# Kernel optimization log

Measured on AMD Instinct MI355X. Metric: run time of the kernel, lower is better.

Reference implementation:

```python
import jax, jax.numpy as jnp
import numpy as np

B, T, D, H, E = 2, 1024, 1024, 4096, 8


def setup_inputs() -> dict:
    key = jax.random.key(0)
    ks = jax.random.split(key, 7)
    s = 0.02  # weight init scale
    return {
        "x": jax.random.normal(ks[0], (B, T, D), jnp.float32),
        "gate_w": jax.random.normal(ks[1], (D, E), jnp.float32) * s,
        "gate_b": jnp.zeros((E,), jnp.float32),
        "w1": jax.random.normal(ks[2], (E, D, H), jnp.float32) * s,
        "b1": jnp.zeros((E, H), jnp.float32),
        "w2": jax.random.normal(ks[3], (E, H, D), jnp.float32) * s,
        "b2": jnp.zeros((E, D), jnp.float32),
    }


def reference(x, gate_w, gate_b, w1, b1, w2, b2):
    b, t, d = x.shape
    e = gate_w.shape[1]
    xt = x.reshape(b * t, d)                      # [N, D]
    logits = xt @ gate_w + gate_b                 # [N, E]
    probs = jax.nn.softmax(logits, axis=-1)
    top_expert = jnp.argmax(probs, axis=-1)       # [N]
    onehot = jax.nn.one_hot(top_expert, e, dtype=x.dtype)  # [N, E]
    # dense per-expert FFN, then combine via top-1 one-hot (same math as masked dispatch)
    h = jax.nn.gelu(jnp.einsum('nd,edh->enh', xt, w1) + b1[:, None, :], approximate=False)  # [E, N, H]
    y = jnp.einsum('enh,ehd->end', h, w2) + b2[:, None, :]                                  # [E, N, D]
    out = jnp.einsum('end,ne->nd', y, onehot).reshape(b, t, d)
    counts = jnp.sum(onehot, axis=0)              # [E], float
    frac = counts / jnp.maximum(counts.sum(), 1.0)
    aux_loss = jnp.mean((frac - 1.0 / e) ** 2)
    return out, aux_loss
```

## Files before the change

### kernel.cpp

```cpp
#include <hip/hip_runtime.h>
#include <stdint.h>

#define N_TOK 2048
#define DDIM 1024
#define HDIM 4096
#define NEXP 8
#define BM 128
#define MAXT 24
#define PADCAP 3072

#define C_COUNTS 0
#define C_CURSOR 8
#define C_PADOFF 16
#define C_TILECNT 25
#define C_TILE_E 32
#define C_TILE_M0 56
#define C_TILE_ROWS 80
#define C_EXPERT 128
#define C_PERM 2176

#define XG_OFF 32768
#define HG_OFF (XG_OFF + PADCAP*DDIM*2)

typedef float f32x4 __attribute__((ext_vector_type(4)));
typedef short s16x8 __attribute__((ext_vector_type(8)));
typedef unsigned int u32;
typedef unsigned short u16;

__device__ __forceinline__ u16 f2bf(float f){
  u32 u = __float_as_uint(f);
  u += 0x7fffu + ((u >> 16) & 1u);
  return (u16)(u >> 16);
}

__device__ __forceinline__ u32 pkbf(float a, float b){
  u32 r; asm("v_cvt_pk_bf16_f32 %0, %1, %2" : "=v"(r) : "v"(a), "v"(b)); return r;
}

__device__ __forceinline__ void gl_lds16(const void* g, void* l){
  __builtin_amdgcn_global_load_lds((const __attribute__((address_space(1))) u32*)g,
                                   (__attribute__((address_space(3))) u32*)l, 16, 0, 0);
}

__global__ __launch_bounds__(256) void gate_kern(
    const float* __restrict__ x, const float* __restrict__ gw,
    const float* __restrict__ gb, int* __restrict__ ctrl)
{
  const int wv = threadIdx.x >> 6, l = threadIdx.x & 63;
  const int n = blockIdx.x * 4 + wv;
  const float* xr = x + (size_t)n * DDIM;
  float acc[NEXP];
  #pragma unroll
  for (int e = 0; e < NEXP; e++) acc[e] = 0.f;
  #pragma unroll 4
  for (int i = 0; i < DDIM/64; i++){
    int k = i*64 + l;
    float xv = xr[k];
    const float* g = gw + (size_t)k * NEXP;
    #pragma unroll
    for (int e = 0; e < NEXP; e++) acc[e] = fmaf(xv, g[e], acc[e]);
  }
  #pragma unroll
  for (int e = 0; e < NEXP; e++){
    #pragma unroll
    for (int off = 32; off > 0; off >>= 1) acc[e] += __shfl_xor(acc[e], off);
  }
  if (l == 0){
    float best = acc[0] + gb[0]; int bi = 0;
    #pragma unroll
    for (int e = 1; e < NEXP; e++){
      float v = acc[e] + gb[e];
      if (v > best){ best = v; bi = e; }
    }
    ctrl[C_EXPERT + n] = bi;
    atomicAdd(&ctrl[C_COUNTS + bi], 1);
  }
}

__global__ void setup_kern(int* __restrict__ ctrl, float* __restrict__ aux_out)
{
  const int t = threadIdx.x;
  for (int i = t; i < PADCAP; i += 256) ctrl[C_PERM + i] = -1;
  if (t == 0){
    int off = 0, tc = 0;
    float aux = 0.f;
    for (int e = 0; e < NEXP; e++){
      int c = ctrl[C_COUNTS + e];
      ctrl[C_PADOFF + e] = off;
      ctrl[C_CURSOR + e] = off;
      int nt = (c + BM - 1) / BM;
      for (int j = 0; j < nt; j++){
        ctrl[C_TILE_E   + tc] = e;
        ctrl[C_TILE_M0  + tc] = off + j*BM;
        ctrl[C_TILE_ROWS+ tc] = min(BM, c - j*BM);
        tc++;
      }
      off += nt * BM;
      float fr = (float)c * (1.f/(float)N_TOK);
      float d = fr - 1.f/(float)NEXP;
      aux += d*d;
    }
    ctrl[C_TILECNT] = tc;
    *aux_out = aux * (1.f/(float)NEXP);
  }
}

__global__ __launch_bounds__(256) void scatter_kern(int* __restrict__ ctrl)
{
  const int n = blockIdx.x * 256 + threadIdx.x;
  const int e = ctrl[C_EXPERT + n];
  const int pos = atomicAdd(&ctrl[C_CURSOR + e], 1);
  ctrl[C_PERM + pos] = n;
}

__global__ __launch_bounds__(256) void xg_kern(
    const float* __restrict__ x, const int* __restrict__ ctrl,
    u16* __restrict__ Xg)
{
  const int slot = blockIdx.x, t = threadIdx.x;
  const int tok = ctrl[C_PERM + slot];
  ushort4 o;
  if (tok >= 0){
    f32x4 v = *(const f32x4*)(x + (size_t)tok*DDIM + t*4);
    o.x = f2bf(v.x); o.y = f2bf(v.y); o.z = f2bf(v.z); o.w = f2bf(v.w);
  } else { o.x = 0; o.y = 0; o.z = 0; o.w = 0; }
  *(ushort4*)(Xg + (size_t)slot*DDIM + t*4) = o;
}

template<int MODE>
__global__ __launch_bounds__(256, (MODE==1) ? 3 : 2) void moe_gemm(
    const u16* __restrict__ Ag, const float* __restrict__ W,
    const float* __restrict__ bias, u16* __restrict__ Hg,
    float* __restrict__ outp, const int* __restrict__ ctrl)
{
  constexpr int K    = (MODE==1) ? DDIM : HDIM;
  constexpr int NN   = (MODE==1) ? HDIM : DDIM;
  constexpr int BN   = (MODE==1) ? 128 : 64;
  constexpr int BK   = (MODE==1) ? 32 : 64;
  constexpr int NF   = BN / 32;
  constexpr int NKK  = BK / 32;
  constexpr int CPR  = BK / 8;
  constexpr int AVM  = (BM*BK)/(256*8);
  constexpr int BCPR = BN / 4;
  constexpr int BVM  = (BK*BN)/(256*4);
  constexpr int NT   = K / BK;

  const int by = blockIdx.y;
  if (by >= ctrl[C_TILECNT]) return;
  const int e    = ctrl[C_TILE_E + by];
  const int m0   = ctrl[C_TILE_M0 + by];
  const int rows = ctrl[C_TILE_ROWS + by];
  const int n0   = blockIdx.x * BN;

  const int tid = threadIdx.x;
  const int w = tid >> 6, l = tid & 63;
  const int wr = w >> 1, wc = w & 1;
  const int lhi = l >> 4, llo = l & 15;

  __shared__ __align__(16) u16   As[2][BM*BK];
  __shared__ __align__(16) float Bs[2][BK*BN];
  __shared__ int perm_s[BM];

  if constexpr (MODE == 2){
    if (tid < BM) perm_s[tid] = ctrl[C_PERM + m0 + tid];
  }

  f32x4 acc[4][NF];
  #pragma unroll
  for (int mf = 0; mf < 4; mf++)
    #pragma unroll
    for (int nf = 0; nf < NF; nf++) acc[mf][nf] = (f32x4){0.f,0.f,0.f,0.f};

  const u16* Abase = Ag + (size_t)m0 * K;
  int arow[AVM], apos[AVM];
  #pragma unroll
  for (int i = 0; i < AVM; i++){
    int f = i*256 + tid;
    arow[i] = f / CPR;
    apos[i] = (f & (CPR-1)) ^ (arow[i] & (CPR-1));
  }
  const float* Wb = W + (size_t)e * K * NN + n0;
  int brow[BVM], bpos[BVM];
  #pragma unroll
  for (int i = 0; i < BVM; i++){
    int f = i*256 + tid;
    brow[i] = f / BCPR;
    bpos[i] = (f % BCPR) ^ (((brow[i] >> 3) & 1) << 2);
  }

  const int col0 = wc*(BN/2) + llo;
  const int bswz = (lhi & 1) << 2;

#define STAGE_A(buf, k0) { \
    u16* ad = &As[buf][(w*64)*8]; \
    _Pragma("unroll") \
    for (int i = 0; i < AVM; i++) \
      gl_lds16(Abase + (size_t)arow[i]*K + (k0) + apos[i]*8, ad + i*256*8); }

#define STAGE_B(buf, k0) { \
    float* bd = &Bs[buf][(w*64)*4]; \
    _Pragma("unroll") \
    for (int i = 0; i < BVM; i++) \
      gl_lds16(Wb + (size_t)((k0) + brow[i])*NN + bpos[i]*4, bd + i*256*4); }

#define COMPUTE(buf) { \
    _Pragma("unroll") \
    for (int kk = 0; kk < NKK; kk++){ \
      s16x8 a[4]; \
      _Pragma("unroll") \
      for (int mf = 0; mf < 4; mf++){ \
        int row = wr*64 + mf*16 + llo; \
        int pos = ((kk<<2) | lhi) ^ (row & (CPR-1)); \
        a[mf] = *(const s16x8*)&As[buf][row*BK + pos*8]; } \
      _Pragma("unroll") \
      for (int nf = 0; nf < NF; nf++){ \
        const int col = col0 + nf*16; \
        const float* bp_ = &Bs[buf][(kk*32 + lhi*8)*BN + \
                                    ((((col) >> 2) ^ bswz) << 2) + ((col) & 3)]; \
        union { u32 u[4]; s16x8 v; } bb_; \
        bb_.u[0] = pkbf(bp_[0*BN], bp_[1*BN]); \
        bb_.u[1] = pkbf(bp_[2*BN], bp_[3*BN]); \
        bb_.u[2] = pkbf(bp_[4*BN], bp_[5*BN]); \
        bb_.u[3] = pkbf(bp_[6*BN], bp_[7*BN]); \
        _Pragma("unroll") \
        for (int mf = 0; mf < 4; mf++) \
          acc[mf][nf] = __builtin_amdgcn_mfma_f32_16x16x32_bf16(a[mf], bb_.v, acc[mf][nf], 0, 0, 0); \
      } } }

  STAGE_A(0, 0);
  STAGE_B(0, 0);
  __syncthreads();

  int cur = 0;
  #pragma unroll 1
  for (int t = 0; t < NT; t++){
    if (t+1 < NT){
      STAGE_A(cur^1, (t+1)*BK);
      STAGE_B(cur^1, (t+1)*BK);
    }
    COMPUTE(cur);
    __syncthreads();
    cur ^= 1;
  }

  if constexpr (MODE == 1){
    const float* bp = bias + (size_t)e*NN + n0;
    #pragma unroll
    for (int nf = 0; nf < NF; nf++){
      const int cl = wc*(BN/2) + nf*16 + llo;
      const float bb = bp[cl];
      #pragma unroll
      for (int mf = 0; mf < 4; mf++){
        #pragma unroll
        for (int r = 0; r < 4; r++){
          const int rl = wr*64 + mf*16 + lhi*4 + r;
          float vv = acc[mf][nf][r] + bb;
          float gel = 0.5f * vv * (1.0f + erff(vv * 0.70710678118f));
          Hg[(size_t)(m0+rl)*NN + n0 + cl] = f2bf(gel);
        }
      }
    }
  } else {
    const float* bp = bias + (size_t)e*NN + n0;
    #pragma unroll
    for (int mf = 0; mf < 4; mf++){
      #pragma unroll
      for (int r = 0; r < 4; r++){
        const int rl = wr*64 + mf*16 + lhi*4 + r;
        if (rl < rows){
          const int tok = perm_s[rl];
          #pragma unroll
          for (int nf = 0; nf < NF; nf++){
            const int cl = wc*(BN/2) + nf*16 + llo;
            outp[(size_t)tok*DDIM + n0 + cl] = acc[mf][nf][r] + bp[cl];
          }
        }
      }
    }
  }
#undef STAGE_A
#undef STAGE_B
#undef COMPUTE
}

extern "C" void kernel_launch(void* const* d_in, const int* in_sizes, int n_in,
                              void* d_out, int out_size, void* d_ws, size_t ws_size,
                              hipStream_t stream)
{
  (void)in_sizes; (void)n_in; (void)out_size; (void)ws_size;
  const float* x  = (const float*)d_in[0];
  const float* gw = (const float*)d_in[1];
  const float* gb = (const float*)d_in[2];
  const float* w1 = (const float*)d_in[3];
  const float* b1 = (const float*)d_in[4];
  const float* w2 = (const float*)d_in[5];
  const float* b2 = (const float*)d_in[6];
  float* out = (float*)d_out;
  char* ws = (char*)d_ws;
  int* ctrl = (int*)ws;
  u16* Xg = (u16*)(ws + XG_OFF);
  u16* Hg = (u16*)(ws + HG_OFF);

  hipMemsetAsync(ctrl, 0, 64, stream);
  gate_kern<<<N_TOK/4, 256, 0, stream>>>(x, gw, gb, ctrl);
  setup_kern<<<1, 256, 0, stream>>>(ctrl, out + (size_t)N_TOK*DDIM);
  scatter_kern<<<N_TOK/256, 256, 0, stream>>>(ctrl);
  xg_kern<<<PADCAP, 256, 0, stream>>>(x, ctrl, Xg);
  moe_gemm<1><<<dim3(HDIM/128, MAXT), 256, 0, stream>>>(Xg, w1, b1, Hg, nullptr, ctrl);
  moe_gemm<2><<<dim3(DDIM/64,  MAXT), 256, 0, stream>>>(Hg, w2, b2, nullptr, out, ctrl);
}
```

Baseline: 207.9 us.

## Split-K the second expert GEMM with atomics and shrink tiles for more blocks

After: 238.4 us. +14.7%, slower.

```diff
diff --git a/kernel.cpp b/kernel.cpp
--- a/kernel.cpp
+++ b/kernel.cpp
@@ -128,22 +128,23 @@
 }
 
 template<int MODE>
-__global__ __launch_bounds__(256, (MODE==1) ? 3 : 2) void moe_gemm(
+__global__ __launch_bounds__(256, 4) void moe_gemm(
     const u16* __restrict__ Ag, const float* __restrict__ W,
     const float* __restrict__ bias, u16* __restrict__ Hg,
     float* __restrict__ outp, const int* __restrict__ ctrl)
 {
   constexpr int K    = (MODE==1) ? DDIM : HDIM;
   constexpr int NN   = (MODE==1) ? HDIM : DDIM;
-  constexpr int BN   = (MODE==1) ? 128 : 64;
-  constexpr int BK   = (MODE==1) ? 32 : 64;
+  constexpr int KS   = (MODE==1) ? 1 : 4;
+  constexpr int KLOC = K / KS;
+  constexpr int BN   = 64;
+  constexpr int BK   = 32;
   constexpr int NF   = BN / 32;
-  constexpr int NKK  = BK / 32;
   constexpr int CPR  = BK / 8;
   constexpr int AVM  = (BM*BK)/(256*8);
   constexpr int BCPR = BN / 4;
   constexpr int BVM  = (BK*BN)/(256*4);
-  constexpr int NT   = K / BK;
+  constexpr int NT   = KLOC / BK;
 
   const int by = blockIdx.y;
   if (by >= ctrl[C_TILECNT]) return;
@@ -151,6 +152,7 @@
   const int m0   = ctrl[C_TILE_M0 + by];
   const int rows = ctrl[C_TILE_ROWS + by];
   const int n0   = blockIdx.x * BN;
+  const int kb   = (MODE==1) ? 0 : blockIdx.z * KLOC;
 
   const int tid = threadIdx.x;
   const int w = tid >> 6, l = tid & 63;
@@ -204,39 +206,37 @@
       gl_lds16(Wb + (size_t)((k0) + brow[i])*NN + bpos[i]*4, bd + i*256*4); }
 
 #define COMPUTE(buf) { \
+    s16x8 a[4]; \
     _Pragma("unroll") \
-    for (int kk = 0; kk < NKK; kk++){ \
-      s16x8 a[4]; \
+    for (int mf = 0; mf < 4; mf++){ \
+      int row = wr*64 + mf*16 + llo; \
+      int pos = lhi ^ (row & (CPR-1)); \
+      a[mf] = *(const s16x8*)&As[buf][row*BK + pos*8]; } \
+    _Pragma("unroll") \
+    for (int nf = 0; nf < NF; nf++){ \
+      const int col = col0 + nf*16; \
+      const float* bp_ = &Bs[buf][(lhi*8)*BN + \
+                                  ((((col) >> 2) ^ bswz) << 2) + ((col) & 3)]; \
+      union { u32 u[4]; s16x8 v; } bb_; \
+      bb_.u[0] = pkbf(bp_[0*BN], bp_[1*BN]); \
+      bb_.u[1] = pkbf(bp_[2*BN], bp_[3*BN]); \
+      bb_.u[2] = pkbf(bp_[4*BN], bp_[5*BN]); \
+      bb_.u[3] = pkbf(bp_[6*BN], bp_[7*BN]); \
       _Pragma("unroll") \
-      for (int mf = 0; mf < 4; mf++){ \
-        int row = wr*64 + mf*16 + llo; \
-        int pos = ((kk<<2) | lhi) ^ (row & (CPR-1)); \
-        a[mf] = *(const s16x8*)&As[buf][row*BK + pos*8]; } \
-      _Pragma("unroll") \
-      for (int nf = 0; nf < NF; nf++){ \
-        const int col = col0 + nf*16; \
-        const float* bp_ = &Bs[buf][(kk*32 + lhi*8)*BN + \
-                                    ((((col) >> 2) ^ bswz) << 2) + ((col) & 3)]; \
-        union { u32 u[4]; s16x8 v; } bb_; \
-        bb_.u[0] = pkbf(bp_[0*BN], bp_[1*BN]); \
-        bb_.u[1] = pkbf(bp_[2*BN], bp_[3*BN]); \
-        bb_.u[2] = pkbf(bp_[4*BN], bp_[5*BN]); \
-        bb_.u[3] = pkbf(bp_[6*BN], bp_[7*BN]); \
-        _Pragma("unroll") \
-        for (int mf = 0; mf < 4; mf++) \
-          acc[mf][nf] = __builtin_amdgcn_mfma_f32_16x16x32_bf16(a[mf], bb_.v, acc[mf][nf], 0, 0, 0); \
-      } } }
-
-  STAGE_A(0, 0);
-  STAGE_B(0, 0);
+      for (int mf = 0; mf < 4; mf++) \
+        acc[mf][nf] = __builtin_amdgcn_mfma_f32_16x16x32_bf16(a[mf], bb_.v, acc[mf][nf], 0, 0, 0); \
+    } }
+
+  STAGE_A(0, kb);
+  STAGE_B(0, kb);
   __syncthreads();
 
   int cur = 0;
   #pragma unroll 1
   for (int t = 0; t < NT; t++){
     if (t+1 < NT){
-      STAGE_A(cur^1, (t+1)*BK);
-      STAGE_B(cur^1, (t+1)*BK);
+      STAGE_A(cur^1, kb + (t+1)*BK);
+      STAGE_B(cur^1, kb + (t+1)*BK);
     }
     COMPUTE(cur);
     __syncthreads();
@@ -262,6 +262,7 @@
     }
   } else {
     const float* bp = bias + (size_t)e*NN + n0;
+    const bool addb = (blockIdx.z == 0);
     #pragma unroll
     for (int mf = 0; mf < 4; mf++){
       #pragma unroll
@@ -272,7 +273,8 @@
           #pragma unroll
           for (int nf = 0; nf < NF; nf++){
             const int cl = wc*(BN/2) + nf*16 + llo;
-            outp[(size_t)tok*DDIM + n0 + cl] = acc[mf][nf][r] + bp[cl];
+            float v = acc[mf][nf][r] + (addb ? bp[cl] : 0.f);
+            atomicAdd(&outp[(size_t)tok*DDIM + n0 + cl], v);
           }
         }
       }
@@ -302,10 +304,11 @@
   u16* Hg = (u16*)(ws + HG_OFF);
 
   hipMemsetAsync(ctrl, 0, 64, stream);
+  hipMemsetAsync(out, 0, (size_t)N_TOK*DDIM*4, stream);
   gate_kern<<<N_TOK/4, 256, 0, stream>>>(x, gw, gb, ctrl);
   setup_kern<<<1, 256, 0, stream>>>(ctrl, out + (size_t)N_TOK*DDIM);
   scatter_kern<<<N_TOK/256, 256, 0, stream>>>(ctrl);
   xg_kern<<<PADCAP, 256, 0, stream>>>(x, ctrl, Xg);
-  moe_gemm<1><<<dim3(HDIM/128, MAXT), 256, 0, stream>>>(Xg, w1, b1, Hg, nullptr, ctrl);
-  moe_gemm<2><<<dim3(DDIM/64,  MAXT), 256, 0, stream>>>(Hg, w2, b2, nullptr, out, ctrl);
-}
+  moe_gemm<1><<<dim3(HDIM/64, MAXT),    256, 0, stream>>>(Xg, w1, b1, Hg, nullptr, ctrl);
+  moe_gemm<2><<<dim3(DDIM/64, MAXT, 4), 256, 0, stream>>>(Hg, w2, b2, nullptr, out, ctrl);
+}
```
